# Optimization experiments

Measured on AMD Instinct MI355X. Metric: run time of the kernel, lower is better.

The kernel has to match this reference:

```python
import jax, jax.numpy as jnp
import numpy as np

BS, C, H, W = 64, 3, 512, 512
DROP_PIX = 0.3          # fraction of pixels dropped
NOISE_STD = 0.1         # gaussian multiplicative noise std
RNG_SEED = 42           # internal forward randomness (torch RNG analog)


def setup_inputs() -> dict:
    key = jax.random.key(0)
    x = jax.random.normal(key, (BS, C, H, W), dtype=jnp.float32)
    return {"x": x}


def reference(x):
    bs, c, h, w = x.shape
    hw = h * w
    len_keep = int(hw * (1.0 - DROP_PIX))
    k_mask, k_noise = jax.random.split(jax.random.key(RNG_SEED))

    # Per-sample random permutation of pixel indices, keep first len_keep.
    # argsort of iid uniforms == uniformly random permutation (all bs at once,
    # replacing the Python loop + per-iteration randperm of the original).
    u = jax.random.uniform(k_mask, (bs, hw))
    keep_idx = jnp.argsort(u, axis=1)[:, :len_keep]          # [bs, len_keep]
    mask = jnp.zeros((bs, hw), dtype=x.dtype)
    mask = mask.at[jnp.arange(bs)[:, None], keep_idx].set(1.0)
    mask = mask.reshape(bs, 1, h, w)

    # drop_type == 'zeros'
    x = x * mask

    # additive_noise: gaussian multiplicative noise (real-valued branch)
    noise = jax.random.normal(k_noise, x.shape, dtype=x.dtype) * NOISE_STD + 1.0
    x = x * noise
    return x, mask
```

## Files before the change

### kernel.cpp

```cpp
#include <hip/hip_runtime.h>
#include <hip/hip_bf16.h>

typedef unsigned int u32;
typedef unsigned long long u64;

__host__ __device__ __forceinline__ void tf2x32(u32 k0, u32 k1, u32 x0, u32 x1,
                                                u32& o0, u32& o1)
{
    const u32 ks2 = k0 ^ k1 ^ 0x1BD11BDAu;
    x0 += k0; x1 += k1;
#define TF_R(r) { x0 += x1; x1 = (x1 << (r)) | (x1 >> (32 - (r))); x1 ^= x0; }
    TF_R(13) TF_R(15) TF_R(26) TF_R(6)
    x0 += k1; x1 += ks2 + 1u;
    TF_R(17) TF_R(29) TF_R(16) TF_R(24)
    x0 += ks2; x1 += k0 + 2u;
    TF_R(13) TF_R(15) TF_R(26) TF_R(6)
    x0 += k0; x1 += k1 + 3u;
    TF_R(17) TF_R(29) TF_R(16) TF_R(24)
    x0 += k1; x1 += ks2 + 4u;
    TF_R(13) TF_R(15) TF_R(26) TF_R(6)
    x0 += ks2; x1 += k0 + 5u;
#undef TF_R
    o0 = x0; o1 = x1;
}

__device__ __forceinline__ u32 rbits(u32 k0, u32 k1, u32 e)
{
    u32 o0, o1; tf2x32(k0, k1, 0u, e, o0, o1); return o0 ^ o1;
}

#define HW        262144u
#define PMASK     262143u
#define KEEP      183500u
#define NX        50331648u
#define NM        16777216u
#define LO_F      (-0.99999994039535522461f)

__device__ __forceinline__ float noise_from_bits(u32 bits)
{
    float f  = __uint_as_float((bits >> 9) | 0x3F800000u) - 1.0f;
    float un = fmaf(f, 2.0f, LO_F);
    un = fmaxf(LO_F, un);
    float w = -__logf(fmaf(-un, un, 1.0f));
    float p;
    if (w < 5.0f) {
        w -= 2.5f;
        p = 2.81022636e-08f;
        p = fmaf(p, w, 3.43273939e-07f);
        p = fmaf(p, w, -3.5233877e-06f);
        p = fmaf(p, w, -4.39150654e-06f);
        p = fmaf(p, w, 0.00021858087f);
        p = fmaf(p, w, -0.00125372503f);
        p = fmaf(p, w, -0.00417768164f);
        p = fmaf(p, w, 0.246640727f);
        p = fmaf(p, w, 1.50140941f);
    } else {
        w = __fsqrt_rn(w) - 3.0f;
        p = -0.000200214257f;
        p = fmaf(p, w, 0.000100950558f);
        p = fmaf(p, w, 0.00134934322f);
        p = fmaf(p, w, -0.00367342844f);
        p = fmaf(p, w, 0.00573950773f);
        p = fmaf(p, w, -0.0076224613f);
        p = fmaf(p, w, 0.00943887047f);
        p = fmaf(p, w, 1.00167406f);
        p = fmaf(p, w, 2.83297682f);
    }
    float ei = p * un;
    return fmaf(1.41421356f * ei, 0.1f, 1.0f);
}

__global__ __launch_bounds__(256) void k1_gen_hist(u32 mk0, u32 mk1, u32* mbuf, u32* hist)
{
    __shared__ u32 lh[4096];
    const int t = threadIdx.x;
    const u32 blk = blockIdx.x;
    const u32 row = blk >> 4;
    const u32 base = blk << 14;
#pragma unroll
    for (int i = 0; i < 16; ++i) lh[t + (i << 8)] = 0;
    __syncthreads();
    uint4* mv = (uint4*)mbuf;
#pragma unroll 1
    for (int i = 0; i < 16; ++i) {
        u32 vi = (u32)(i << 8) + (u32)t;
        u32 e = base + (vi << 2);
        uint4 q;
        q.x = rbits(mk0, mk1, e)     >> 9;
        q.y = rbits(mk0, mk1, e + 1) >> 9;
        q.z = rbits(mk0, mk1, e + 2) >> 9;
        q.w = rbits(mk0, mk1, e + 3) >> 9;
        mv[(base >> 2) + vi] = q;
        atomicAdd(&lh[q.x >> 11], 1u);
        atomicAdd(&lh[q.y >> 11], 1u);
        atomicAdd(&lh[q.z >> 11], 1u);
        atomicAdd(&lh[q.w >> 11], 1u);
    }
    __syncthreads();
    u32* gh = hist + (row << 12);
#pragma unroll
    for (int i = 0; i < 16; ++i) {
        u32 idx = (u32)t + (i << 8);
        u32 v = lh[idx];
        if (v) atomicAdd(&gh[idx], v);
    }
}

template <int PER>
__device__ __forceinline__ void rank_scan(const u32* h, u32 k, u32* sh, u32& bin, u32& rem)
{
    const int t = threadIdx.x;
    u32 v[PER]; u32 s = 0;
#pragma unroll
    for (int i = 0; i < PER; ++i) { v[i] = h[t * PER + i]; s += v[i]; }
    sh[t] = s;
    __syncthreads();
    if (t == 0) {
        u32 run = 0; u32 c = 0;
        for (; c < 255u; ++c) { u32 cs = sh[c]; if (run + cs >= k) break; run += cs; }
        sh[256] = c; sh[257] = run;
    }
    __syncthreads();
    u32 c = sh[256];
    if (t == (int)c) {
        u32 run = sh[257];
        u32 b = (u32)t * PER + PER - 1; u32 r = k - run;
#pragma unroll
        for (int i = 0; i < PER; ++i) {
            if (run + v[i] >= k) { b = (u32)t * PER + i; r = k - run; break; }
            run += v[i];
        }
        sh[256] = b; sh[257] = r;
    }
    __syncthreads();
    bin = sh[256]; rem = sh[257];
    __syncthreads();
}

__global__ __launch_bounds__(256) void k2b_finehist(const u32* mbuf, const u32* hist,
                                                    u32* fhist, u32* rowBr)
{
    __shared__ u32 sh[258];
    __shared__ u32 fh[2048];
    const int t = threadIdx.x;
    const u32 blk = blockIdx.x;
    const u32 row = blk >> 4;
    u32 B, r;
    rank_scan<16>(hist + (row << 12), KEEP, sh, B, r);
    if ((blk & 15u) == 0 && t == 0) { rowBr[row * 2] = B; rowBr[row * 2 + 1] = r; }
#pragma unroll
    for (int i = 0; i < 8; ++i) fh[t + (i << 8)] = 0;
    __syncthreads();
    const uint4* mv = (const uint4*)mbuf + (blk << 12);
#pragma unroll 1
    for (int i = 0; i < 16; ++i) {
        uint4 q = mv[(i << 8) + t];
        if ((q.x >> 11) == B) atomicAdd(&fh[q.x & 2047u], 1u);
        if ((q.y >> 11) == B) atomicAdd(&fh[q.y & 2047u], 1u);
        if ((q.z >> 11) == B) atomicAdd(&fh[q.z & 2047u], 1u);
        if ((q.w >> 11) == B) atomicAdd(&fh[q.w & 2047u], 1u);
    }
    __syncthreads();
    u32* gf = fhist + (row << 11);
#pragma unroll
    for (int i = 0; i < 8; ++i) {
        u32 idx = (u32)t + (i << 8);
        u32 v = fh[idx];
        if (v) atomicAdd(&gf[idx], v);
    }
}

__global__ __launch_bounds__(256) void k2d_ties(const u32* mbuf, const u32* fhist,
                                                const u32* rowBr, u32* rowM,
                                                u32* tiecnt, u32* tielist)
{
    __shared__ u32 sh[258];
    const int t = threadIdx.x;
    const u32 blk = blockIdx.x;
    const u32 row = blk >> 4;
    u32 r = rowBr[row * 2 + 1];
    u32 B = rowBr[row * 2];
    u32 f, r2;
    rank_scan<8>(fhist + (row << 11), r, sh, f, r2);
    u32 mstar = (B << 11) | f;
    if ((blk & 15u) == 0 && t == 0) { rowM[row * 2] = mstar; rowM[row * 2 + 1] = r2; }
    const uint4* mv = (const uint4*)mbuf + (blk << 12);
#pragma unroll 1
    for (int i = 0; i < 16; ++i) {
        u32 vi = (u32)(i << 8) + (u32)t;
        uint4 q = mv[vi];
        u32 p = ((blk & 15u) << 14) + (vi << 2);
        if (q.x == mstar) { u32 pos = atomicAdd(&tiecnt[row], 1u); if (pos < 256u) tielist[(row << 8) + pos] = p; }
        if (q.y == mstar) { u32 pos = atomicAdd(&tiecnt[row], 1u); if (pos < 256u) tielist[(row << 8) + pos] = p + 1; }
        if (q.z == mstar) { u32 pos = atomicAdd(&tiecnt[row], 1u); if (pos < 256u) tielist[(row << 8) + pos] = p + 2; }
        if (q.w == mstar) { u32 pos = atomicAdd(&tiecnt[row], 1u); if (pos < 256u) tielist[(row << 8) + pos] = p + 3; }
    }
}

__global__ __launch_bounds__(64) void k2e_select(const u32* rowM, const u32* tiecnt,
                                                 const u32* tielist, u64* rowsel)
{
    __shared__ u32 list[256];
    const int t = threadIdx.x;
    const u32 row = blockIdx.x;
    u32 mstar = rowM[row * 2], r2 = rowM[row * 2 + 1];
    u32 cnt = tiecnt[row]; if (cnt > 256u) cnt = 256u;
    for (u32 i = (u32)t; i < cnt; i += 64u) list[i] = tielist[(row << 8) + i];
    __syncthreads();
    if (t == 0) {
        if (r2 > cnt) r2 = cnt;
        u32 pstar = 0;
        for (u32 it = 0; it < r2; ++it) {
            u32 mn = 0xFFFFFFFFu, mi = 0;
            for (u32 i2 = 0; i2 < cnt; ++i2) if (list[i2] < mn) { mn = list[i2]; mi = i2; }
            pstar = mn; list[mi] = 0xFFFFFFFFu;
        }
        rowsel[row] = ((u64)mstar << 18) | (u64)pstar;
    }
}

__global__ __launch_bounds__(256) void k3_mask(u32* mbuf, const u64* rowsel)
{
    u32 tid = blockIdx.x * 256u + threadIdx.x;
    u32 row = tid >> 16;
    u64 kst = rowsel[row];
    uint4 q = ((const uint4*)mbuf)[tid];
    u32 p = (tid << 2) & PMASK;
    float4 o;
    o.x = ((((u64)q.x << 18) | (u64)(p))     <= kst) ? 1.0f : 0.0f;
    o.y = ((((u64)q.y << 18) | (u64)(p + 1)) <= kst) ? 1.0f : 0.0f;
    o.z = ((((u64)q.z << 18) | (u64)(p + 2)) <= kst) ? 1.0f : 0.0f;
    o.w = ((((u64)q.w << 18) | (u64)(p + 3)) <= kst) ? 1.0f : 0.0f;
    ((float4*)mbuf)[tid] = o;
}

__global__ __launch_bounds__(256) void k4_final(const float4* x4, const float* maskf,
                                                float4* out4, u32 nk0, u32 nk1)
{
    u32 tid = blockIdx.x * 256u + threadIdx.x;
    u32 e = tid << 2;
    u32 b = e / 786432u;
    u32 p = e & PMASK;
    float4 mk = *(const float4*)(maskf + ((b << 18) | p));
    float4 xv = x4[tid];
    float4 r;
    r.x = (xv.x * mk.x) * noise_from_bits(rbits(nk0, nk1, e));
    r.y = (xv.y * mk.y) * noise_from_bits(rbits(nk0, nk1, e + 1));
    r.z = (xv.z * mk.z) * noise_from_bits(rbits(nk0, nk1, e + 2));
    r.w = (xv.w * mk.w) * noise_from_bits(rbits(nk0, nk1, e + 3));
    out4[tid] = r;
}

extern "C" void kernel_launch(void* const* d_in, const int* in_sizes, int n_in,
                              void* d_out, int out_size, void* d_ws, size_t ws_size,
                              hipStream_t stream) {
    const float* x = (const float*)d_in[0];
    float* xout = (float*)d_out;
    u32*  outu = (u32*)d_out;
    u32*  mbuf = (u32*)(xout + NX);

    u32* hist    = outu;
    u32* fhist   = outu + 262144;
    u32* tiecnt  = outu + 393216;
    u32* tielist = outu + 393472;
    u32* rowBr   = outu + 409856;
    u32* rowM    = outu + 410112;
    u64* rowsel  = (u64*)(outu + 410368);

    u32 mk0, mk1, nk0, nk1;
    tf2x32(0u, 42u, 0u, 0u, mk0, mk1);
    tf2x32(0u, 42u, 0u, 1u, nk0, nk1);

    hipMemsetAsync(hist, 0, (262144u + 131072u + 64u) * sizeof(u32), stream);
    k1_gen_hist<<<1024, 256, 0, stream>>>(mk0, mk1, mbuf, hist);
    k2b_finehist<<<1024, 256, 0, stream>>>(mbuf, hist, fhist, rowBr);
    k2d_ties<<<1024, 256, 0, stream>>>(mbuf, fhist, rowBr, rowM, tiecnt, tielist);
    k2e_select<<<64, 64, 0, stream>>>(rowM, tiecnt, tielist, rowsel);
    k3_mask<<<16384, 256, 0, stream>>>(mbuf, rowsel);
    k4_final<<<49152, 256, 0, stream>>>((const float4*)x, (const float*)mbuf,
                                        (float4*)xout, nk0, nk1);
    (void)d_ws; (void)ws_size; (void)in_sizes; (void)n_in; (void)out_size;
}
```

Baseline: 514.6 us.

## Restructure top-k mask pipeline into per-row select kernel and fused mask+noise pass

Replaces the six-kernel pipeline (gen+hist, fine hist, ties, select, mask, final) and its memset with three kernels. Random generation now runs as a standalone elementwise kernel. One 1024-thread block per row does the coarse histogram, gathers candidates in the boundary bin into shared memory, and finds the k-th element by rank counting. The mask build is fused with the noise multiply, so each mask value is reused across the three channels. This removes global atomics, several launches and a mask round-trip. In exchange, only 64 blocks run the select phase, which may underuse the GPU, and the candidate list is capped at 512 entries.

```diff
diff --git a/kernel.cpp b/kernel.cpp
--- a/kernel.cpp
+++ b/kernel.cpp
@@ -70,185 +70,120 @@
     return fmaf(1.41421356f * ei, 0.1f, 1.0f);
 }
 
-__global__ __launch_bounds__(256) void k1_gen_hist(u32 mk0, u32 mk1, u32* mbuf, u32* hist)
-{
-    __shared__ u32 lh[4096];
+__global__ __launch_bounds__(256) void k1_gen(u32 mk0, u32 mk1, uint4* mv)
+{
+    u32 tid = blockIdx.x * 256u + threadIdx.x;
+    u32 e = tid << 2;
+    uint4 q;
+    q.x = rbits(mk0, mk1, e)      >> 9;
+    q.y = rbits(mk0, mk1, e + 1u) >> 9;
+    q.z = rbits(mk0, mk1, e + 2u) >> 9;
+    q.w = rbits(mk0, mk1, e + 3u) >> 9;
+    mv[tid] = q;
+}
+
+__global__ __launch_bounds__(1024) void k2_select(const u32* mbuf, u64* rowsel)
+{
+    __shared__ u32 hist[4096];
+    __shared__ u32 sh[1026];
+    __shared__ u32 cand[512];
+    __shared__ u32 ccnt;
     const int t = threadIdx.x;
-    const u32 blk = blockIdx.x;
-    const u32 row = blk >> 4;
-    const u32 base = blk << 14;
+    const u32 row = blockIdx.x;
+    const uint4* mv = (const uint4*)mbuf + ((u64)row << 16);
+
+    for (int i = t; i < 4096; i += 1024) hist[i] = 0;
+    if (t == 0) ccnt = 0;
+    __syncthreads();
+
+#pragma unroll 1
+    for (int i = 0; i < 64; ++i) {
+        uint4 q = mv[(i << 10) + t];
+        atomicAdd(&hist[q.x >> 11], 1u);
+        atomicAdd(&hist[q.y >> 11], 1u);
+        atomicAdd(&hist[q.z >> 11], 1u);
+        atomicAdd(&hist[q.w >> 11], 1u);
+    }
+    __syncthreads();
+
+    u32 v0 = hist[t * 4], v1 = hist[t * 4 + 1], v2 = hist[t * 4 + 2], v3 = hist[t * 4 + 3];
+    sh[t] = v0 + v1 + v2 + v3;
+    __syncthreads();
+    if (t == 0) {
+        u32 run = 0, c = 0;
+        for (; c < 1023u; ++c) { u32 cs = sh[c]; if (run + cs >= KEEP) break; run += cs; }
+        sh[1024] = c; sh[1025] = run;
+    }
+    __syncthreads();
+    u32 c = sh[1024];
+    if (t == (int)c) {
+        u32 run = sh[1025];
+        u32 v[4] = { v0, v1, v2, v3 };
+        u32 b = (u32)t * 4u + 3u, r = KEEP - run;
 #pragma unroll
-    for (int i = 0; i < 16; ++i) lh[t + (i << 8)] = 0;
-    __syncthreads();
-    uint4* mv = (uint4*)mbuf;
-#pragma unroll 1
-    for (int i = 0; i < 16; ++i) {
-        u32 vi = (u32)(i << 8) + (u32)t;
-        u32 e = base + (vi << 2);
-        uint4 q;
-        q.x = rbits(mk0, mk1, e)     >> 9;
-        q.y = rbits(mk0, mk1, e + 1) >> 9;
-        q.z = rbits(mk0, mk1, e + 2) >> 9;
-        q.w = rbits(mk0, mk1, e + 3) >> 9;
-        mv[(base >> 2) + vi] = q;
-        atomicAdd(&lh[q.x >> 11], 1u);
-        atomicAdd(&lh[q.y >> 11], 1u);
-        atomicAdd(&lh[q.z >> 11], 1u);
-        atomicAdd(&lh[q.w >> 11], 1u);
-    }
-    __syncthreads();
-    u32* gh = hist + (row << 12);
-#pragma unroll
-    for (int i = 0; i < 16; ++i) {
-        u32 idx = (u32)t + (i << 8);
-        u32 v = lh[idx];
-        if (v) atomicAdd(&gh[idx], v);
-    }
-}
-
-template <int PER>
-__device__ __forceinline__ void rank_scan(const u32* h, u32 k, u32* sh, u32& bin, u32& rem)
-{
-    const int t = threadIdx.x;
-    u32 v[PER]; u32 s = 0;
-#pragma unroll
-    for (int i = 0; i < PER; ++i) { v[i] = h[t * PER + i]; s += v[i]; }
-    sh[t] = s;
-    __syncthreads();
-    if (t == 0) {
-        u32 run = 0; u32 c = 0;
-        for (; c < 255u; ++c) { u32 cs = sh[c]; if (run + cs >= k) break; run += cs; }
-        sh[256] = c; sh[257] = run;
-    }
-    __syncthreads();
-    u32 c = sh[256];
-    if (t == (int)c) {
-        u32 run = sh[257];
-        u32 b = (u32)t * PER + PER - 1; u32 r = k - run;
-#pragma unroll
-        for (int i = 0; i < PER; ++i) {
-            if (run + v[i] >= k) { b = (u32)t * PER + i; r = k - run; break; }
+        for (int i = 0; i < 4; ++i) {
+            if (run + v[i] >= KEEP) { b = (u32)t * 4u + (u32)i; r = KEEP - run; break; }
             run += v[i];
         }
-        sh[256] = b; sh[257] = r;
-    }
-    __syncthreads();
-    bin = sh[256]; rem = sh[257];
-    __syncthreads();
-}
-
-__global__ __launch_bounds__(256) void k2b_finehist(const u32* mbuf, const u32* hist,
-                                                    u32* fhist, u32* rowBr)
-{
-    __shared__ u32 sh[258];
-    __shared__ u32 fh[2048];
-    const int t = threadIdx.x;
-    const u32 blk = blockIdx.x;
-    const u32 row = blk >> 4;
-    u32 B, r;
-    rank_scan<16>(hist + (row << 12), KEEP, sh, B, r);
-    if ((blk & 15u) == 0 && t == 0) { rowBr[row * 2] = B; rowBr[row * 2 + 1] = r; }
+        sh[1024] = b; sh[1025] = r;
+    }
+    __syncthreads();
+    const u32 B = sh[1024];
+    const u32 r = sh[1025];
+    __syncthreads();
+
+#pragma unroll 1
+    for (int i = 0; i < 64; ++i) {
+        u32 vi = (u32)(i << 10) + (u32)t;
+        uint4 q = mv[vi];
+        u32 p = vi << 2;
+        if ((q.x >> 11) == B) { u32 pos = atomicAdd(&ccnt, 1u); if (pos < 512u) cand[pos] = ((q.x & 2047u) << 18) | p; }
+        if ((q.y >> 11) == B) { u32 pos = atomicAdd(&ccnt, 1u); if (pos < 512u) cand[pos] = ((q.y & 2047u) << 18) | (p + 1u); }
+        if ((q.z >> 11) == B) { u32 pos = atomicAdd(&ccnt, 1u); if (pos < 512u) cand[pos] = ((q.z & 2047u) << 18) | (p + 2u); }
+        if ((q.w >> 11) == B) { u32 pos = atomicAdd(&ccnt, 1u); if (pos < 512u) cand[pos] = ((q.w & 2047u) << 18) | (p + 3u); }
+    }
+    __syncthreads();
+
+    u32 cnt = ccnt; if (cnt > 512u) cnt = 512u;
+    if ((u32)t < cnt) {
+        u32 me = cand[t];
+        u32 rk = 0;
+        for (u32 j = 0; j < cnt; ++j) rk += (cand[j] < me) ? 1u : 0u;
+        if (rk == r - 1u) {
+            u32 mstar = (B << 11) | (me >> 18);
+            rowsel[row] = ((u64)mstar << 18) | (u64)(me & 0x3FFFFu);
+        }
+    }
+}
+
+__global__ __launch_bounds__(256) void k3_fused(const float4* x4, u32* mmask,
+                                                const u64* rowsel, float4* out4,
+                                                u32 nk0, u32 nk1)
+{
+    u32 tid = blockIdx.x * 256u + threadIdx.x;
+    u32 b  = tid >> 16;
+    u32 pq = tid & 65535u;
+    u32 p  = pq << 2;
+    u64 kst = rowsel[b];
+    uint4 q = ((const uint4*)mmask)[tid];
+    float4 mk;
+    mk.x = ((((u64)q.x << 18) | (u64)p)        <= kst) ? 1.0f : 0.0f;
+    mk.y = ((((u64)q.y << 18) | (u64)(p + 1u)) <= kst) ? 1.0f : 0.0f;
+    mk.z = ((((u64)q.z << 18) | (u64)(p + 2u)) <= kst) ? 1.0f : 0.0f;
+    mk.w = ((((u64)q.w << 18) | (u64)(p + 3u)) <= kst) ? 1.0f : 0.0f;
 #pragma unroll
-    for (int i = 0; i < 8; ++i) fh[t + (i << 8)] = 0;
-    __syncthreads();
-    const uint4* mv = (const uint4*)mbuf + (blk << 12);
-#pragma unroll 1
-    for (int i = 0; i < 16; ++i) {
-        uint4 q = mv[(i << 8) + t];
-        if ((q.x >> 11) == B) atomicAdd(&fh[q.x & 2047u], 1u);
-        if ((q.y >> 11) == B) atomicAdd(&fh[q.y & 2047u], 1u);
-        if ((q.z >> 11) == B) atomicAdd(&fh[q.z & 2047u], 1u);
-        if ((q.w >> 11) == B) atomicAdd(&fh[q.w & 2047u], 1u);
-    }
-    __syncthreads();
-    u32* gf = fhist + (row << 11);
-#pragma unroll
-    for (int i = 0; i < 8; ++i) {
-        u32 idx = (u32)t + (i << 8);
-        u32 v = fh[idx];
-        if (v) atomicAdd(&gf[idx], v);
-    }
-}
-
-__global__ __launch_bounds__(256) void k2d_ties(const u32* mbuf, const u32* fhist,
-                                                const u32* rowBr, u32* rowM,
-                                                u32* tiecnt, u32* tielist)
-{
-    __shared__ u32 sh[258];
-    const int t = threadIdx.x;
-    const u32 blk = blockIdx.x;
-    const u32 row = blk >> 4;
-    u32 r = rowBr[row * 2 + 1];
-    u32 B = rowBr[row * 2];
-    u32 f, r2;
-    rank_scan<8>(fhist + (row << 11), r, sh, f, r2);
-    u32 mstar = (B << 11) | f;
-    if ((blk & 15u) == 0 && t == 0) { rowM[row * 2] = mstar; rowM[row * 2 + 1] = r2; }
-    const uint4* mv = (const uint4*)mbuf + (blk << 12);
-#pragma unroll 1
-    for (int i = 0; i < 16; ++i) {
-        u32 vi = (u32)(i << 8) + (u32)t;
-        uint4 q = mv[vi];
-        u32 p = ((blk & 15u) << 14) + (vi << 2);
-        if (q.x == mstar) { u32 pos = atomicAdd(&tiecnt[row], 1u); if (pos < 256u) tielist[(row << 8) + pos] = p; }
-        if (q.y == mstar) { u32 pos = atomicAdd(&tiecnt[row], 1u); if (pos < 256u) tielist[(row << 8) + pos] = p + 1; }
-        if (q.z == mstar) { u32 pos = atomicAdd(&tiecnt[row], 1u); if (pos < 256u) tielist[(row << 8) + pos] = p + 2; }
-        if (q.w == mstar) { u32 pos = atomicAdd(&tiecnt[row], 1u); if (pos < 256u) tielist[(row << 8) + pos] = p + 3; }
-    }
-}
-
-__global__ __launch_bounds__(64) void k2e_select(const u32* rowM, const u32* tiecnt,
-                                                 const u32* tielist, u64* rowsel)
-{
-    __shared__ u32 list[256];
-    const int t = threadIdx.x;
-    const u32 row = blockIdx.x;
-    u32 mstar = rowM[row * 2], r2 = rowM[row * 2 + 1];
-    u32 cnt = tiecnt[row]; if (cnt > 256u) cnt = 256u;
-    for (u32 i = (u32)t; i < cnt; i += 64u) list[i] = tielist[(row << 8) + i];
-    __syncthreads();
-    if (t == 0) {
-        if (r2 > cnt) r2 = cnt;
-        u32 pstar = 0;
-        for (u32 it = 0; it < r2; ++it) {
-            u32 mn = 0xFFFFFFFFu, mi = 0;
-            for (u32 i2 = 0; i2 < cnt; ++i2) if (list[i2] < mn) { mn = list[i2]; mi = i2; }
-            pstar = mn; list[mi] = 0xFFFFFFFFu;
-        }
-        rowsel[row] = ((u64)mstar << 18) | (u64)pstar;
-    }
-}
-
-__global__ __launch_bounds__(256) void k3_mask(u32* mbuf, const u64* rowsel)
-{
-    u32 tid = blockIdx.x * 256u + threadIdx.x;
-    u32 row = tid >> 16;
-    u64 kst = rowsel[row];
-    uint4 q = ((const uint4*)mbuf)[tid];
-    u32 p = (tid << 2) & PMASK;
-    float4 o;
-    o.x = ((((u64)q.x << 18) | (u64)(p))     <= kst) ? 1.0f : 0.0f;
-    o.y = ((((u64)q.y << 18) | (u64)(p + 1)) <= kst) ? 1.0f : 0.0f;
-    o.z = ((((u64)q.z << 18) | (u64)(p + 2)) <= kst) ? 1.0f : 0.0f;
-    o.w = ((((u64)q.w << 18) | (u64)(p + 3)) <= kst) ? 1.0f : 0.0f;
-    ((float4*)mbuf)[tid] = o;
-}
-
-__global__ __launch_bounds__(256) void k4_final(const float4* x4, const float* maskf,
-                                                float4* out4, u32 nk0, u32 nk1)
-{
-    u32 tid = blockIdx.x * 256u + threadIdx.x;
-    u32 e = tid << 2;
-    u32 b = e / 786432u;
-    u32 p = e & PMASK;
-    float4 mk = *(const float4*)(maskf + ((b << 18) | p));
-    float4 xv = x4[tid];
-    float4 r;
-    r.x = (xv.x * mk.x) * noise_from_bits(rbits(nk0, nk1, e));
-    r.y = (xv.y * mk.y) * noise_from_bits(rbits(nk0, nk1, e + 1));
-    r.z = (xv.z * mk.z) * noise_from_bits(rbits(nk0, nk1, e + 2));
-    r.w = (xv.w * mk.w) * noise_from_bits(rbits(nk0, nk1, e + 3));
-    out4[tid] = r;
+    for (u32 ch = 0; ch < 3u; ++ch) {
+        u32 xi = ((b * 3u + ch) << 16) + pq;
+        u32 e  = ((b * 3u + ch) << 18) + p;
+        float4 xv = x4[xi];
+        float4 rr;
+        rr.x = (xv.x * mk.x) * noise_from_bits(rbits(nk0, nk1, e));
+        rr.y = (xv.y * mk.y) * noise_from_bits(rbits(nk0, nk1, e + 1u));
+        rr.z = (xv.z * mk.z) * noise_from_bits(rbits(nk0, nk1, e + 2u));
+        rr.w = (xv.w * mk.w) * noise_from_bits(rbits(nk0, nk1, e + 3u));
+        out4[xi] = rr;
+    }
+    ((float4*)mmask)[tid] = mk;
 }
 
 extern "C" void kernel_launch(void* const* d_in, const int* in_sizes, int n_in,
@@ -256,28 +191,16 @@
                               hipStream_t stream) {
     const float* x = (const float*)d_in[0];
     float* xout = (float*)d_out;
-    u32*  outu = (u32*)d_out;
-    u32*  mbuf = (u32*)(xout + NX);
-
-    u32* hist    = outu;
-    u32* fhist   = outu + 262144;
-    u32* tiecnt  = outu + 393216;
-    u32* tielist = outu + 393472;
-    u32* rowBr   = outu + 409856;
-    u32* rowM    = outu + 410112;
-    u64* rowsel  = (u64*)(outu + 410368);
+    u32*  mmask = (u32*)(xout + NX);
+    u64*  rowsel = (u64*)d_ws;
 
     u32 mk0, mk1, nk0, nk1;
     tf2x32(0u, 42u, 0u, 0u, mk0, mk1);
     tf2x32(0u, 42u, 0u, 1u, nk0, nk1);
 
-    hipMemsetAsync(hist, 0, (262144u + 131072u + 64u) * sizeof(u32), stream);
-    k1_gen_hist<<<1024, 256, 0, stream>>>(mk0, mk1, mbuf, hist);
-    k2b_finehist<<<1024, 256, 0, stream>>>(mbuf, hist, fhist, rowBr);
-    k2d_ties<<<1024, 256, 0, stream>>>(mbuf, fhist, rowBr, rowM, tiecnt, tielist);
-    k2e_select<<<64, 64, 0, stream>>>(rowM, tiecnt, tielist, rowsel);
-    k3_mask<<<16384, 256, 0, stream>>>(mbuf, rowsel);
-    k4_final<<<49152, 256, 0, stream>>>((const float4*)x, (const float*)mbuf,
+    k1_gen<<<16384, 256, 0, stream>>>(mk0, mk1, (uint4*)mmask);
+    k2_select<<<64, 1024, 0, stream>>>(mmask, rowsel);
+    k3_fused<<<16384, 256, 0, stream>>>((const float4*)x, mmask, rowsel,
                                         (float4*)xout, nk0, nk1);
     (void)d_ws; (void)ws_size; (void)in_sizes; (void)n_in; (void)out_size;
 }
```

Result: slower. 527.0 us (+2.4%).
